# Performance work log

Measured on AMD Instinct MI355X. Metric: run time of the kernel, lower is better.

The kernel has to match this reference:

```python
import jax, jax.numpy as jnp
import numpy as np

N = 50000      # num nodes
E = 500000     # num edges
IN = 128       # in_dim
H = 8          # num_heads
D = 16         # h_dim (out_dim)
CLAMP = 5.0

def setup_inputs() -> dict:
    key = jax.random.key(0)
    ks = jax.random.split(key, 12)
    def xavier(k, shape, fan_in, fan_out):
        std = float(np.sqrt(2.0 / (fan_in + fan_out)))
        return jax.random.normal(k, shape, dtype=jnp.float32) * std
    return {
        "x": jax.random.normal(ks[0], (N, IN), dtype=jnp.float32),
        "edge_attr": jax.random.normal(ks[1], (E, IN), dtype=jnp.float32),
        "edge_index": jax.random.randint(ks[2], (2, E), 0, N, dtype=jnp.int32),
        # Linear weights stored as [in, out] for x @ W + b
        "WQ": xavier(ks[3], (IN, H * D), IN, H * D),
        "bQ": jnp.zeros((H * D,), jnp.float32),
        "WK": xavier(ks[4], (IN, H * D), IN, H * D),
        "bK": jnp.zeros((H * D,), jnp.float32),
        "WE": xavier(ks[5], (IN, 2 * H * D), IN, 2 * H * D),
        "bE": jnp.zeros((2 * H * D,), jnp.float32),
        "WV": xavier(ks[6], (IN, H * D), IN, H * D),
        "bV": jnp.zeros((H * D,), jnp.float32),
        "Aw": xavier(ks[7], (D, H, 1), D, 1),
        "VeRow": xavier(ks[8], (D, H, D), D, D),
    }

def reference(x, edge_attr, edge_index, WQ, bQ, WK, bK, WE, bE, WV, bV, Aw, VeRow):
    src, dst = edge_index[0], edge_index[1]
    Qh = (x @ WQ + bQ).reshape(N, H, D)
    Kh = (x @ WK + bK).reshape(N, H, D)
    Vh = (x @ WV + bV).reshape(N, H, D)
    Ex = (edge_attr @ WE + bE).reshape(E, H, 2 * D)

    # additive score: gathered K/Q plus signed-sqrt edge term
    score1 = Kh[src] + Qh[dst]                       # [E,H,D]
    s2 = Ex[:, :, :D] * Ex[:, :, D:]
    score2 = jnp.sqrt(jax.nn.relu(s2)) - jnp.sqrt(jax.nn.relu(-s2))
    conn = score1 + score2                           # act = Identity

    score = jnp.einsum('ehd,dhc->ehc', conn, Aw)     # [E,H,1]
    score = jnp.clip(score, -CLAMP, CLAMP)

    # scatter-softmax over destination nodes
    m = jax.ops.segment_max(score, dst, num_segments=N)      # [N,H,1]
    ex = jnp.exp(score - m[dst])
    denom = jax.ops.segment_sum(ex, dst, num_segments=N)
    attn = ex / (denom[dst] + 1e-16)                 # [E,H,1]

    # weighted scatter-add aggregation
    msg = Vh[src] * attn                             # [E,H,D]
    Vo = Qh + jax.ops.segment_sum(msg, dst, num_segments=N)
    rowV = jax.ops.segment_sum(conn * attn, dst, num_segments=N)
    Vo = Vo + jnp.einsum('nhd,dhc->nhc', rowV, VeRow)

    return Vo.reshape(N, H * D), conn.reshape(E, H * D)
```

## Files before the change

kernel.cpp:

```cpp
#include <hip/hip_runtime.h>
#include <math.h>

#define N_NODES 50000
#define N_EDGES 500000
#define IN_DIM  128
#define NH      8
#define HD      16
#define OUTD    128
#define CLAMP_V 5.0f

__global__ __launch_bounds__(256) void node_gemm_kernel(
    const float* __restrict__ x,
    const float* __restrict__ WQ, const float* __restrict__ bQ,
    const float* __restrict__ WK, const float* __restrict__ bK,
    const float* __restrict__ WV, const float* __restrict__ bV,
    float* __restrict__ Vo, float* __restrict__ Kh, float* __restrict__ Vh)
{
    __shared__ float A[64][132];
    __shared__ float B[64][64];

    const int t  = threadIdx.x;
    const int bx = blockIdx.x;
    const int by = blockIdx.y;
    const int which = by >> 1;
    const int ch    = (by & 1) * 64;

    const float* W    = (which == 0) ? WQ : (which == 1 ? WK : WV);
    const float* bias = (which == 0) ? bQ : (which == 1 ? bK : bV);
    float*       out  = (which == 0) ? Vo : (which == 1 ? Kh : Vh);

    const int r0 = bx * 64;

    #pragma unroll
    for (int it = 0; it < 8; ++it) {
        int idx = it * 256 + t;
        int k4  = idx & 31;
        int r   = idx >> 5;
        float4 v = make_float4(0.f, 0.f, 0.f, 0.f);
        if (r0 + r < N_NODES)
            v = *(const float4*)(x + (size_t)(r0 + r) * IN_DIM + k4 * 4);
        *(float4*)&A[r][k4 * 4] = v;
    }

    const int tx = t & 15, ty = t >> 4;
    float acc[4][4] = {};

    for (int kh = 0; kh < 2; ++kh) {
        __syncthreads();
        #pragma unroll
        for (int it = 0; it < 4; ++it) {
            int idx = it * 256 + t;
            int c4  = idx & 15;
            int kk  = idx >> 4;
            float4 v = *(const float4*)(W + (size_t)(kh * 64 + kk) * 128 + ch + c4 * 4);
            *(float4*)&B[kk][c4 * 4] = v;
        }
        __syncthreads();

        #pragma unroll 4
        for (int k = 0; k < 64; k += 4) {
            float4 a4[4], b4[4];
            a4[0] = *(const float4*)&A[ty * 4 + 0][kh * 64 + k];
            a4[1] = *(const float4*)&A[ty * 4 + 1][kh * 64 + k];
            a4[2] = *(const float4*)&A[ty * 4 + 2][kh * 64 + k];
            a4[3] = *(const float4*)&A[ty * 4 + 3][kh * 64 + k];
            b4[0] = *(const float4*)&B[k + 0][tx * 4];
            b4[1] = *(const float4*)&B[k + 1][tx * 4];
            b4[2] = *(const float4*)&B[k + 2][tx * 4];
            b4[3] = *(const float4*)&B[k + 3][tx * 4];
            const float* aa = (const float*)a4;
            const float* bb = (const float*)b4;
            #pragma unroll
            for (int kk = 0; kk < 4; ++kk)
                #pragma unroll
                for (int i = 0; i < 4; ++i)
                    #pragma unroll
                    for (int j = 0; j < 4; ++j)
                        acc[i][j] += aa[i * 4 + kk] * bb[kk * 4 + j];
        }
    }

    #pragma unroll
    for (int i = 0; i < 4; ++i) {
        int r = r0 + ty * 4 + i;
        if (r < N_NODES) {
            #pragma unroll
            for (int j = 0; j < 4; ++j) {
                int c = ch + tx * 4 + j;
                out[(size_t)r * OUTD + c] = acc[i][j] + bias[c];
            }
        }
    }
}

__global__ __launch_bounds__(256) void edge_kernel(
    const float* __restrict__ edge_attr,
    const int*   __restrict__ edge_index,
    const float* __restrict__ WE, const float* __restrict__ bE,
    const float* __restrict__ Aw,
    const float* __restrict__ Qh,
    const float* __restrict__ Kh,
    float* __restrict__ conn_out,
    float* __restrict__ exp_s,
    float* __restrict__ denom)
{
    __shared__ float A[64][132];
    __shared__ float B[64][64];

    const int t  = threadIdx.x;
    const int e0 = blockIdx.x * 64;
    const int c0 = blockIdx.y * 64;

    #pragma unroll
    for (int it = 0; it < 8; ++it) {
        int idx = it * 256 + t;
        int k4  = idx & 31;
        int r   = idx >> 5;
        float4 v = make_float4(0.f, 0.f, 0.f, 0.f);
        if (e0 + r < N_EDGES)
            v = *(const float4*)(edge_attr + (size_t)(e0 + r) * IN_DIM + k4 * 4);
        *(float4*)&A[r][k4 * 4] = v;
    }

    const int tx = t & 15, ty = t >> 4;
    float acc[4][4] = {};

    for (int kh = 0; kh < 2; ++kh) {
        __syncthreads();
        #pragma unroll
        for (int it = 0; it < 4; ++it) {
            int idx = it * 256 + t;
            int c4  = idx & 15;
            int kk  = idx >> 4;
            float4 v = *(const float4*)(WE + (size_t)(kh * 64 + kk) * 256 + c0 + c4 * 4);
            *(float4*)&B[kk][c4 * 4] = v;
        }
        __syncthreads();

        #pragma unroll 4
        for (int k = 0; k < 64; k += 4) {
            float4 a4[4], b4[4];
            a4[0] = *(const float4*)&A[ty * 4 + 0][kh * 64 + k];
            a4[1] = *(const float4*)&A[ty * 4 + 1][kh * 64 + k];
            a4[2] = *(const float4*)&A[ty * 4 + 2][kh * 64 + k];
            a4[3] = *(const float4*)&A[ty * 4 + 3][kh * 64 + k];
            b4[0] = *(const float4*)&B[k + 0][tx * 4];
            b4[1] = *(const float4*)&B[k + 1][tx * 4];
            b4[2] = *(const float4*)&B[k + 2][tx * 4];
            b4[3] = *(const float4*)&B[k + 3][tx * 4];
            const float* aa = (const float*)a4;
            const float* bb = (const float*)b4;
            #pragma unroll
            for (int kk = 0; kk < 4; ++kk)
                #pragma unroll
                for (int i = 0; i < 4; ++i)
                    #pragma unroll
                    for (int j = 0; j < 4; ++j)
                        acc[i][j] += aa[i * 4 + kk] * bb[kk * 4 + j];
        }
    }
    __syncthreads();

    #pragma unroll
    for (int i = 0; i < 4; ++i)
        #pragma unroll
        for (int j = 0; j < 4; ++j)
            A[ty * 4 + i][tx * 4 + j] = acc[i][j] + bE[c0 + tx * 4 + j];
    __syncthreads();

    if (t < 128) {
        const int r  = t >> 1;
        const int hl = t & 1;
        const int e  = e0 + r;
        if (e < N_EDGES) {
            const int h   = (c0 >> 5) + hl;
            const int src = edge_index[e];
            const int dst = edge_index[N_EDGES + e];

            const float4* K4 = (const float4*)(Kh + (size_t)src * OUTD + h * HD);
            const float4* Q4 = (const float4*)(Qh + (size_t)dst * OUTD + h * HD);
            float kq[16];
            #pragma unroll
            for (int i = 0; i < 4; ++i) {
                float4 kk = K4[i], qq = Q4[i];
                kq[i * 4 + 0] = kk.x + qq.x;
                kq[i * 4 + 1] = kk.y + qq.y;
                kq[i * 4 + 2] = kk.z + qq.z;
                kq[i * 4 + 3] = kk.w + qq.w;
            }

            float cv[16];
            float score = 0.f;
            #pragma unroll
            for (int d = 0; d < 16; ++d) {
                float s2 = A[r][hl * 32 + d] * A[r][hl * 32 + 16 + d];
                float sq = (s2 >= 0.f) ? sqrtf(s2) : -sqrtf(-s2);
                float c  = kq[d] + sq;
                cv[d] = c;
                score += c * Aw[d * NH + h];
            }
            float4* co = (float4*)(conn_out + (size_t)e * OUTD + h * HD);
            #pragma unroll
            for (int i = 0; i < 4; ++i)
                co[i] = make_float4(cv[i * 4 + 0], cv[i * 4 + 1],
                                    cv[i * 4 + 2], cv[i * 4 + 3]);

            score = fminf(fmaxf(score, -CLAMP_V), CLAMP_V);
            float ex = expf(score);
            exp_s[(size_t)e * NH + h] = ex;
            atomicAdd(&denom[(size_t)dst * NH + h], ex);
        }
    }
}

__global__ __launch_bounds__(256) void scatter_kernel(
    const int*   __restrict__ edge_index,
    const float* __restrict__ Vh,
    const float* __restrict__ conn,
    const float* __restrict__ exp_s,
    const float* __restrict__ denom,
    float* __restrict__ Vo,
    float* __restrict__ rowV)
{
    const int t = threadIdx.x;
    const int e = blockIdx.x * 2 + (t >> 7);
    const int c = t & 127;
    const int h = c >> 4;

    const int src = edge_index[e];
    const int dst = edge_index[N_EDGES + e];

    const float attn = exp_s[(size_t)e * NH + h] /
                       (denom[(size_t)dst * NH + h] + 1e-16f);

    const float mv = Vh[(size_t)src * OUTD + c] * attn;
    atomicAdd(&Vo[(size_t)dst * OUTD + c], mv);
    const float rv = conn[(size_t)e * OUTD + c] * attn;
    atomicAdd(&rowV[(size_t)dst * OUTD + c], rv);
}

__global__ __launch_bounds__(256) void finalize_kernel(
    const float* __restrict__ rowV,
    const float* __restrict__ VeRow,
    float* __restrict__ Vo)
{
    __shared__ float ver[2048];
    __shared__ float rv[256];
    const int t = threadIdx.x;

    #pragma unroll
    for (int it = 0; it < 2; ++it) {
        int idx = it * 256 + t;
        *(float4*)&ver[idx * 4] = *(const float4*)&VeRow[idx * 4];
    }
    const int n0 = blockIdx.x * 2;
    if (t < 64)
        *(float4*)&rv[t * 4] = *(const float4*)&rowV[(size_t)n0 * OUTD + t * 4];
    __syncthreads();

    const int nl = t >> 7, c = t & 127, h = c >> 4, cc = c & 15;
    float acc = 0.f;
    #pragma unroll
    for (int d = 0; d < 16; ++d)
        acc += rv[nl * 128 + h * 16 + d] * ver[d * 128 + h * 16 + cc];

    Vo[(size_t)(n0 + nl) * OUTD + c] += acc;
}

extern "C" void kernel_launch(void* const* d_in, const int* in_sizes, int n_in,
                              void* d_out, int out_size, void* d_ws, size_t ws_size,
                              hipStream_t stream)
{
    const float* x         = (const float*)d_in[0];
    const float* edge_attr = (const float*)d_in[1];
    const int*   edge_index= (const int*)  d_in[2];
    const float* WQ = (const float*)d_in[3];
    const float* bQ = (const float*)d_in[4];
    const float* WK = (const float*)d_in[5];
    const float* bK = (const float*)d_in[6];
    const float* WE = (const float*)d_in[7];
    const float* bE = (const float*)d_in[8];
    const float* WV = (const float*)d_in[9];
    const float* bV = (const float*)d_in[10];
    const float* Aw = (const float*)d_in[11];
    const float* VeRow = (const float*)d_in[12];

    float* Vo   = (float*)d_out;
    float* conn = Vo + (size_t)N_NODES * OUTD;

    float* ws    = (float*)d_ws;
    float* Kh    = ws;
    float* Vh    = Kh   + (size_t)N_NODES * OUTD;
    float* rowV  = Vh   + (size_t)N_NODES * OUTD;
    float* denom = rowV + (size_t)N_NODES * OUTD;
    float* exp_s = denom+ (size_t)N_NODES * NH;

    hipMemsetAsync(rowV,  0, (size_t)N_NODES * OUTD * sizeof(float), stream);
    hipMemsetAsync(denom, 0, (size_t)N_NODES * NH   * sizeof(float), stream);

    dim3 g1((N_NODES + 63) / 64, 6);
    node_gemm_kernel<<<g1, 256, 0, stream>>>(x, WQ, bQ, WK, bK, WV, bV, Vo, Kh, Vh);

    dim3 g2((N_EDGES + 63) / 64, 4);
    edge_kernel<<<g2, 256, 0, stream>>>(edge_attr, edge_index, WE, bE, Aw,
                                        Vo, Kh, conn, exp_s, denom);

    scatter_kernel<<<N_EDGES / 2, 256, 0, stream>>>(edge_index, Vh, conn,
                                                    exp_s, denom, Vo, rowV);

    finalize_kernel<<<N_NODES / 2, 256, 0, stream>>>(rowV, VeRow, Vo);
}
```

Measured before the change: 1.550 ms.

## Use split-bf16 MFMA GEMMs and fuse edge scoring, aggregation and VeRow projection

Replaces the FP32 SIMT GEMMs with MFMA 32x32x16 bf16 GEMMs that use a hi/lo split (three products) to keep near-FP32 accuracy, with weights pre-packed by a small kernel. The edge kernel now covers all 256 edge-projection columns in one block. It also folds the VeRow projection per edge and scatters exp-weighted messages directly, so the scatter and finalize passes and the exp_s/rowV buffers go away. A light final kernel divides by the softmax denominator and adds Q. This trades extra atomics per edge (16 per head) and per-edge VeRow FMAs for removing a full extra pass over conn and Vh gathers. Like before it skips the max subtraction, relying on the clamp.

```diff
diff --git a/kernel.cpp b/kernel.cpp
--- a/kernel.cpp
+++ b/kernel.cpp
@@ -9,177 +9,198 @@
 #define OUTD    128
 #define CLAMP_V 5.0f
 
-__global__ __launch_bounds__(256) void node_gemm_kernel(
+typedef unsigned short ushort_t;
+typedef short bf16x8 __attribute__((ext_vector_type(8)));
+typedef float f32x16 __attribute__((ext_vector_type(16)));
+
+__device__ __forceinline__ ushort_t f2bf(float f) {
+    uint32_t u = __float_as_uint(f);
+    u += 0x7fffu + ((u >> 16) & 1u);
+    return (ushort_t)(u >> 16);
+}
+__device__ __forceinline__ float bf2f(ushort_t h) {
+    return __uint_as_float(((uint32_t)h) << 16);
+}
+
+__device__ __forceinline__ void load_cvt8(const float* p, bool valid,
+                                          bf16x8& hv, bf16x8& lv) {
+    float v[8];
+    if (valid) {
+        float4 a = *(const float4*)p, b = *(const float4*)(p + 4);
+        v[0]=a.x; v[1]=a.y; v[2]=a.z; v[3]=a.w;
+        v[4]=b.x; v[5]=b.y; v[6]=b.z; v[7]=b.w;
+    } else {
+        #pragma unroll
+        for (int j = 0; j < 8; ++j) v[j] = 0.f;
+    }
+    #pragma unroll
+    for (int j = 0; j < 8; ++j) {
+        ushort_t h = f2bf(v[j]);
+        hv[j] = (short)h;
+        lv[j] = (short)f2bf(v[j] - bf2f(h));
+    }
+}
+
+__global__ __launch_bounds__(256) void pack_w_kernel(
+    const float* __restrict__ W, int C,
+    ushort_t* __restrict__ hi, ushort_t* __restrict__ lo)
+{
+    int tid = blockIdx.x * 256 + threadIdx.x;
+    int l  = tid & 63;
+    int ks = (tid >> 6) & 7;
+    int cb = tid >> 9;
+    if (cb * 32 >= C) return;
+    int col = cb * 32 + (l & 31);
+    int k0  = ks * 16 + ((l >> 5) << 3);
+    size_t ob = ((size_t)(cb * 8 + ks) * 64 + l) * 8;
+    #pragma unroll
+    for (int j = 0; j < 8; ++j) {
+        float v = W[(size_t)(k0 + j) * C + col];
+        ushort_t h = f2bf(v);
+        hi[ob + j] = h;
+        lo[ob + j] = f2bf(v - bf2f(h));
+    }
+}
+
+__global__ __launch_bounds__(256) void node_mfma_kernel(
     const float* __restrict__ x,
-    const float* __restrict__ WQ, const float* __restrict__ bQ,
-    const float* __restrict__ WK, const float* __restrict__ bK,
-    const float* __restrict__ WV, const float* __restrict__ bV,
-    float* __restrict__ Vo, float* __restrict__ Kh, float* __restrict__ Vh)
-{
-    __shared__ float A[64][132];
-    __shared__ float B[64][64];
-
-    const int t  = threadIdx.x;
-    const int bx = blockIdx.x;
-    const int by = blockIdx.y;
-    const int which = by >> 1;
-    const int ch    = (by & 1) * 64;
-
-    const float* W    = (which == 0) ? WQ : (which == 1 ? WK : WV);
-    const float* bias = (which == 0) ? bQ : (which == 1 ? bK : bV);
-    float*       out  = (which == 0) ? Vo : (which == 1 ? Kh : Vh);
-
-    const int r0 = bx * 64;
-
-    #pragma unroll
-    for (int it = 0; it < 8; ++it) {
-        int idx = it * 256 + t;
-        int k4  = idx & 31;
-        int r   = idx >> 5;
-        float4 v = make_float4(0.f, 0.f, 0.f, 0.f);
-        if (r0 + r < N_NODES)
-            v = *(const float4*)(x + (size_t)(r0 + r) * IN_DIM + k4 * 4);
-        *(float4*)&A[r][k4 * 4] = v;
-    }
-
-    const int tx = t & 15, ty = t >> 4;
-    float acc[4][4] = {};
-
-    for (int kh = 0; kh < 2; ++kh) {
-        __syncthreads();
-        #pragma unroll
-        for (int it = 0; it < 4; ++it) {
-            int idx = it * 256 + t;
-            int c4  = idx & 15;
-            int kk  = idx >> 4;
-            float4 v = *(const float4*)(W + (size_t)(kh * 64 + kk) * 128 + ch + c4 * 4);
-            *(float4*)&B[kk][c4 * 4] = v;
-        }
-        __syncthreads();
-
-        #pragma unroll 4
-        for (int k = 0; k < 64; k += 4) {
-            float4 a4[4], b4[4];
-            a4[0] = *(const float4*)&A[ty * 4 + 0][kh * 64 + k];
-            a4[1] = *(const float4*)&A[ty * 4 + 1][kh * 64 + k];
-            a4[2] = *(const float4*)&A[ty * 4 + 2][kh * 64 + k];
-            a4[3] = *(const float4*)&A[ty * 4 + 3][kh * 64 + k];
-            b4[0] = *(const float4*)&B[k + 0][tx * 4];
-            b4[1] = *(const float4*)&B[k + 1][tx * 4];
-            b4[2] = *(const float4*)&B[k + 2][tx * 4];
-            b4[3] = *(const float4*)&B[k + 3][tx * 4];
-            const float* aa = (const float*)a4;
-            const float* bb = (const float*)b4;
-            #pragma unroll
-            for (int kk = 0; kk < 4; ++kk)
-                #pragma unroll
-                for (int i = 0; i < 4; ++i)
-                    #pragma unroll
-                    for (int j = 0; j < 4; ++j)
-                        acc[i][j] += aa[i * 4 + kk] * bb[kk * 4 + j];
-        }
-    }
-
-    #pragma unroll
-    for (int i = 0; i < 4; ++i) {
-        int r = r0 + ty * 4 + i;
-        if (r < N_NODES) {
-            #pragma unroll
-            for (int j = 0; j < 4; ++j) {
-                int c = ch + tx * 4 + j;
-                out[(size_t)r * OUTD + c] = acc[i][j] + bias[c];
+    const ushort_t* __restrict__ WQh, const ushort_t* __restrict__ WQl,
+    const ushort_t* __restrict__ WKh, const ushort_t* __restrict__ WKl,
+    const ushort_t* __restrict__ WVh, const ushort_t* __restrict__ WVl,
+    const float* __restrict__ bQ, const float* __restrict__ bK,
+    const float* __restrict__ bV,
+    float* __restrict__ Qs, float* __restrict__ Kn, float* __restrict__ Vn)
+{
+    const int t = threadIdx.x, lane = t & 63, w = t >> 6;
+    const int wi = w >> 1, wjc = w & 1;
+    const int n0 = blockIdx.x * 128;
+    const int which = blockIdx.y;
+    const ushort_t* Whi = (which == 0) ? WQh : (which == 1 ? WKh : WVh);
+    const ushort_t* Wlo = (which == 0) ? WQl : (which == 1 ? WKl : WVl);
+    const float*    bias= (which == 0) ? bQ  : (which == 1 ? bK  : bV);
+    float*          out = (which == 0) ? Qs  : (which == 1 ? Kn  : Vn);
+
+    const int lrow = lane & 31, lk = (lane >> 5) << 3;
+
+    f32x16 acc[2][2];
+    #pragma unroll
+    for (int i = 0; i < 2; ++i)
+        #pragma unroll
+        for (int j = 0; j < 2; ++j)
+            #pragma unroll
+            for (int g = 0; g < 16; ++g) acc[i][j][g] = 0.f;
+
+    #pragma unroll
+    for (int ks = 0; ks < 8; ++ks) {
+        bf16x8 ah[2], al[2];
+        #pragma unroll
+        for (int i = 0; i < 2; ++i) {
+            int row = n0 + wi * 64 + i * 32 + lrow;
+            load_cvt8(x + (size_t)row * IN_DIM + ks * 16 + lk, row < N_NODES,
+                      ah[i], al[i]);
+        }
+        #pragma unroll
+        for (int jf = 0; jf < 2; ++jf) {
+            const int cb = wjc * 2 + jf;
+            size_t ob = ((size_t)(cb * 8 + ks) * 64 + lane) * 8;
+            bf16x8 bh = *(const bf16x8*)(Whi + ob);
+            bf16x8 bl = *(const bf16x8*)(Wlo + ob);
+            #pragma unroll
+            for (int i = 0; i < 2; ++i) {
+                acc[i][jf] = __builtin_amdgcn_mfma_f32_32x32x16_bf16(ah[i], bh, acc[i][jf], 0, 0, 0);
+                acc[i][jf] = __builtin_amdgcn_mfma_f32_32x32x16_bf16(ah[i], bl, acc[i][jf], 0, 0, 0);
+                acc[i][jf] = __builtin_amdgcn_mfma_f32_32x32x16_bf16(al[i], bh, acc[i][jf], 0, 0, 0);
             }
         }
     }
-}
-
-__global__ __launch_bounds__(256) void edge_kernel(
+
+    float bv[2];
+    #pragma unroll
+    for (int jf = 0; jf < 2; ++jf) bv[jf] = bias[wjc * 64 + jf * 32 + lrow];
+
+    #pragma unroll
+    for (int i = 0; i < 2; ++i)
+        #pragma unroll
+        for (int jf = 0; jf < 2; ++jf)
+            #pragma unroll
+            for (int g = 0; g < 16; ++g) {
+                int row = n0 + wi * 64 + i * 32 + (g & 3) + 8 * (g >> 2) + 4 * (lane >> 5);
+                if (row < N_NODES)
+                    out[(size_t)row * OUTD + wjc * 64 + jf * 32 + lrow] = acc[i][jf][g] + bv[jf];
+            }
+}
+
+__global__ __launch_bounds__(256) void edge_mfma_kernel(
     const float* __restrict__ edge_attr,
     const int*   __restrict__ edge_index,
-    const float* __restrict__ WE, const float* __restrict__ bE,
-    const float* __restrict__ Aw,
-    const float* __restrict__ Qh,
-    const float* __restrict__ Kh,
+    const ushort_t* __restrict__ WEh, const ushort_t* __restrict__ WEl,
+    const float* __restrict__ bE, const float* __restrict__ Aw,
+    const float* __restrict__ Qs, const float* __restrict__ Kn,
+    const float* __restrict__ Vn, const float* __restrict__ VeRow,
     float* __restrict__ conn_out,
-    float* __restrict__ exp_s,
+    float* __restrict__ VoAcc,
     float* __restrict__ denom)
 {
-    __shared__ float A[64][132];
-    __shared__ float B[64][64];
-
-    const int t  = threadIdx.x;
+    __shared__ float stash[64 * 256];
+
+    const int t = threadIdx.x, lane = t & 63, w = t >> 6;
+    const int wi = w >> 1, wj = w & 1;
     const int e0 = blockIdx.x * 64;
-    const int c0 = blockIdx.y * 64;
-
-    #pragma unroll
-    for (int it = 0; it < 8; ++it) {
-        int idx = it * 256 + t;
-        int k4  = idx & 31;
-        int r   = idx >> 5;
-        float4 v = make_float4(0.f, 0.f, 0.f, 0.f);
-        if (e0 + r < N_EDGES)
-            v = *(const float4*)(edge_attr + (size_t)(e0 + r) * IN_DIM + k4 * 4);
-        *(float4*)&A[r][k4 * 4] = v;
-    }
-
-    const int tx = t & 15, ty = t >> 4;
-    float acc[4][4] = {};
-
-    for (int kh = 0; kh < 2; ++kh) {
-        __syncthreads();
-        #pragma unroll
-        for (int it = 0; it < 4; ++it) {
-            int idx = it * 256 + t;
-            int c4  = idx & 15;
-            int kk  = idx >> 4;
-            float4 v = *(const float4*)(WE + (size_t)(kh * 64 + kk) * 256 + c0 + c4 * 4);
-            *(float4*)&B[kk][c4 * 4] = v;
-        }
-        __syncthreads();
-
-        #pragma unroll 4
-        for (int k = 0; k < 64; k += 4) {
-            float4 a4[4], b4[4];
-            a4[0] = *(const float4*)&A[ty * 4 + 0][kh * 64 + k];
-            a4[1] = *(const float4*)&A[ty * 4 + 1][kh * 64 + k];
-            a4[2] = *(const float4*)&A[ty * 4 + 2][kh * 64 + k];
-            a4[3] = *(const float4*)&A[ty * 4 + 3][kh * 64 + k];
-            b4[0] = *(const float4*)&B[k + 0][tx * 4];
-            b4[1] = *(const float4*)&B[k + 1][tx * 4];
-            b4[2] = *(const float4*)&B[k + 2][tx * 4];
-            b4[3] = *(const float4*)&B[k + 3][tx * 4];
-            const float* aa = (const float*)a4;
-            const float* bb = (const float*)b4;
-            #pragma unroll
-            for (int kk = 0; kk < 4; ++kk)
-                #pragma unroll
-                for (int i = 0; i < 4; ++i)
-                    #pragma unroll
-                    for (int j = 0; j < 4; ++j)
-                        acc[i][j] += aa[i * 4 + kk] * bb[kk * 4 + j];
-        }
-    }
+
+    const int lrow = lane & 31, lk = (lane >> 5) << 3;
+    const int arow = e0 + wi * 32 + lrow;
+    const bool rvalid = arow < N_EDGES;
+    const float* ap = edge_attr + (size_t)arow * IN_DIM;
+
+    f32x16 acc[4];
+    #pragma unroll
+    for (int jf = 0; jf < 4; ++jf)
+        #pragma unroll
+        for (int g = 0; g < 16; ++g) acc[jf][g] = 0.f;
+
+    #pragma unroll
+    for (int ks = 0; ks < 8; ++ks) {
+        bf16x8 ah, al;
+        load_cvt8(ap + ks * 16 + lk, rvalid, ah, al);
+        #pragma unroll
+        for (int jf = 0; jf < 4; ++jf) {
+            const int cb = wj * 4 + jf;
+            size_t ob = ((size_t)(cb * 8 + ks) * 64 + lane) * 8;
+            bf16x8 bh = *(const bf16x8*)(WEh + ob);
+            bf16x8 bl = *(const bf16x8*)(WEl + ob);
+            acc[jf] = __builtin_amdgcn_mfma_f32_32x32x16_bf16(ah, bh, acc[jf], 0, 0, 0);
+            acc[jf] = __builtin_amdgcn_mfma_f32_32x32x16_bf16(ah, bl, acc[jf], 0, 0, 0);
+            acc[jf] = __builtin_amdgcn_mfma_f32_32x32x16_bf16(al, bh, acc[jf], 0, 0, 0);
+        }
+    }
+
+    float bv[4];
+    #pragma unroll
+    for (int jf = 0; jf < 4; ++jf) bv[jf] = bE[wj * 128 + jf * 32 + lrow];
+    #pragma unroll
+    for (int jf = 0; jf < 4; ++jf)
+        #pragma unroll
+        for (int g = 0; g < 16; ++g) {
+            int r = wi * 32 + (g & 3) + 8 * (g >> 2) + 4 * (lane >> 5);
+            int c = wj * 128 + jf * 32 + lrow;
+            stash[r * 256 + (c ^ (r & 31))] = acc[jf][g] + bv[jf];
+        }
     __syncthreads();
 
-    #pragma unroll
-    for (int i = 0; i < 4; ++i)
-        #pragma unroll
-        for (int j = 0; j < 4; ++j)
-            A[ty * 4 + i][tx * 4 + j] = acc[i][j] + bE[c0 + tx * 4 + j];
-    __syncthreads();
-
-    if (t < 128) {
-        const int r  = t >> 1;
-        const int hl = t & 1;
-        const int e  = e0 + r;
-        if (e < N_EDGES) {
-            const int h   = (c0 >> 5) + hl;
-            const int src = edge_index[e];
-            const int dst = edge_index[N_EDGES + e];
-
-            const float4* K4 = (const float4*)(Kh + (size_t)src * OUTD + h * HD);
-            const float4* Q4 = (const float4*)(Qh + (size_t)dst * OUTD + h * HD);
-            float kq[16];
+    const int r = lane;
+    const int e = e0 + r;
+    const bool valid = e < N_EDGES;
+    const int src = valid ? edge_index[e] : 0;
+    const int dst = valid ? edge_index[N_EDGES + e] : 0;
+
+    #pragma unroll
+    for (int hp = 0; hp < 2; ++hp) {
+        const int h = w + hp * 4;
+
+        float kq[16];
+        {
+            const float4* K4 = (const float4*)(Kn + (size_t)src * OUTD + h * HD);
+            const float4* Q4 = (const float4*)(Qs + (size_t)dst * OUTD + h * HD);
             #pragma unroll
             for (int i = 0; i < 4; ++i) {
                 float4 kk = K4[i], qq = Q4[i];
@@ -188,83 +209,84 @@
                 kq[i * 4 + 2] = kk.z + qq.z;
                 kq[i * 4 + 3] = kk.w + qq.w;
             }
-
-            float cv[16];
-            float score = 0.f;
-            #pragma unroll
-            for (int d = 0; d < 16; ++d) {
-                float s2 = A[r][hl * 32 + d] * A[r][hl * 32 + 16 + d];
-                float sq = (s2 >= 0.f) ? sqrtf(s2) : -sqrtf(-s2);
-                float c  = kq[d] + sq;
-                cv[d] = c;
-                score += c * Aw[d * NH + h];
-            }
+        }
+
+        float cv[16];
+        float score = 0.f;
+        #pragma unroll
+        for (int d = 0; d < 16; ++d) {
+            float x1 = stash[r * 256 + ((h * 32 + d)      ^ (r & 31))];
+            float x2 = stash[r * 256 + ((h * 32 + 16 + d) ^ (r & 31))];
+            float s2 = x1 * x2;
+            float sq = (s2 >= 0.f) ? sqrtf(s2) : -sqrtf(-s2);
+            float c  = kq[d] + sq;
+            cv[d] = c;
+            score += c * Aw[d * NH + h];
+        }
+
+        if (valid) {
             float4* co = (float4*)(conn_out + (size_t)e * OUTD + h * HD);
             #pragma unroll
             for (int i = 0; i < 4; ++i)
                 co[i] = make_float4(cv[i * 4 + 0], cv[i * 4 + 1],
                                     cv[i * 4 + 2], cv[i * 4 + 3]);
-
-            score = fminf(fmaxf(score, -CLAMP_V), CLAMP_V);
-            float ex = expf(score);
-            exp_s[(size_t)e * NH + h] = ex;
-            atomicAdd(&denom[(size_t)dst * NH + h], ex);
-        }
-    }
-}
-
-__global__ __launch_bounds__(256) void scatter_kernel(
-    const int*   __restrict__ edge_index,
-    const float* __restrict__ Vh,
-    const float* __restrict__ conn,
-    const float* __restrict__ exp_s,
-    const float* __restrict__ denom,
-    float* __restrict__ Vo,
-    float* __restrict__ rowV)
-{
-    const int t = threadIdx.x;
-    const int e = blockIdx.x * 2 + (t >> 7);
-    const int c = t & 127;
-    const int h = c >> 4;
-
-    const int src = edge_index[e];
-    const int dst = edge_index[N_EDGES + e];
-
-    const float attn = exp_s[(size_t)e * NH + h] /
-                       (denom[(size_t)dst * NH + h] + 1e-16f);
-
-    const float mv = Vh[(size_t)src * OUTD + c] * attn;
-    atomicAdd(&Vo[(size_t)dst * OUTD + c], mv);
-    const float rv = conn[(size_t)e * OUTD + c] * attn;
-    atomicAdd(&rowV[(size_t)dst * OUTD + c], rv);
-}
-
-__global__ __launch_bounds__(256) void finalize_kernel(
-    const float* __restrict__ rowV,
-    const float* __restrict__ VeRow,
+        }
+
+        score = fminf(fmaxf(score, -CLAMP_V), CLAMP_V);
+        const float ex = __expf(score);
+
+        float outv[16];
+        {
+            const float4* V4 = (const float4*)(Vn + (size_t)src * OUTD + h * HD);
+            #pragma unroll
+            for (int i = 0; i < 4; ++i) {
+                float4 vv = V4[i];
+                outv[i * 4 + 0] = vv.x; outv[i * 4 + 1] = vv.y;
+                outv[i * 4 + 2] = vv.z; outv[i * 4 + 3] = vv.w;
+            }
+        }
+        #pragma unroll
+        for (int d = 0; d < 16; ++d) {
+            const float4* vr = (const float4*)(VeRow + d * OUTD + h * HD);
+            float cvd = cv[d];
+            float4 v0 = vr[0], v1 = vr[1], v2 = vr[2], v3 = vr[3];
+            outv[0]  += cvd * v0.x; outv[1]  += cvd * v0.y;
+            outv[2]  += cvd * v0.z; outv[3]  += cvd * v0.w;
+            outv[4]  += cvd * v1.x; outv[5]  += cvd * v1.y;
+            outv[6]  += cvd * v1.z; outv[7]  += cvd * v1.w;
+            outv[8]  += cvd * v2.x; outv[9]  += cvd * v2.y;
+            outv[10] += cvd * v2.z; outv[11] += cvd * v2.w;
+            outv[12] += cvd * v3.x; outv[13] += cvd * v3.y;
+            outv[14] += cvd * v3.z; outv[15] += cvd * v3.w;
+        }
+
+        if (valid) {
+            atomicAdd(denom + (size_t)dst * NH + h, ex);
+            float* vp = VoAcc + (size_t)dst * OUTD + h * HD;
+            #pragma unroll
+            for (int c = 0; c < 16; ++c)
+                atomicAdd(vp + c, ex * outv[c]);
+        }
+    }
+}
+
+__global__ __launch_bounds__(256) void final_kernel(
+    const float* __restrict__ Qs, const float* __restrict__ denom,
     float* __restrict__ Vo)
 {
-    __shared__ float ver[2048];
-    __shared__ float rv[256];
-    const int t = threadIdx.x;
-
-    #pragma unroll
-    for (int it = 0; it < 2; ++it) {
-        int idx = it * 256 + t;
-        *(float4*)&ver[idx * 4] = *(const float4*)&VeRow[idx * 4];
-    }
-    const int n0 = blockIdx.x * 2;
-    if (t < 64)
-        *(float4*)&rv[t * 4] = *(const float4*)&rowV[(size_t)n0 * OUTD + t * 4];
-    __syncthreads();
-
-    const int nl = t >> 7, c = t & 127, h = c >> 4, cc = c & 15;
-    float acc = 0.f;
-    #pragma unroll
-    for (int d = 0; d < 16; ++d)
-        acc += rv[nl * 128 + h * 16 + d] * ver[d * 128 + h * 16 + cc];
-
-    Vo[(size_t)(n0 + nl) * OUTD + c] += acc;
+    int idx = blockIdx.x * 256 + threadIdx.x;
+    if (idx >= N_NODES * 32) return;
+    int n  = idx >> 5;
+    int c4 = (idx & 31) * 4;
+    int h  = c4 >> 4;
+    float inv = 1.f / (denom[(size_t)n * NH + h] + 1e-16f);
+    float4 a = *(float4*)(Vo + (size_t)n * OUTD + c4);
+    const float4 q = *(const float4*)(Qs + (size_t)n * OUTD + c4);
+    a.x = q.x + a.x * inv;
+    a.y = q.y + a.y * inv;
+    a.z = q.z + a.z * inv;
+    a.w = q.w + a.w * inv;
+    *(float4*)(Vo + (size_t)n * OUTD + c4) = a;
 }
 
 extern "C" void kernel_launch(void* const* d_in, const int* in_sizes, int n_in,
@@ -289,24 +311,35 @@
     float* conn = Vo + (size_t)N_NODES * OUTD;
 
     float* ws    = (float*)d_ws;
-    float* Kh    = ws;
-    float* Vh    = Kh   + (size_t)N_NODES * OUTD;
-    float* rowV  = Vh   + (size_t)N_NODES * OUTD;
-    float* denom = rowV + (size_t)N_NODES * OUTD;
-    float* exp_s = denom+ (size_t)N_NODES * NH;
-
-    hipMemsetAsync(rowV,  0, (size_t)N_NODES * OUTD * sizeof(float), stream);
+    float* Qs    = ws;
+    float* Kn    = Qs + (size_t)N_NODES * OUTD;
+    float* Vn    = Kn + (size_t)N_NODES * OUTD;
+    float* denom = Vn + (size_t)N_NODES * OUTD;
+    ushort_t* WQh = (ushort_t*)(denom + (size_t)N_NODES * NH);
+    ushort_t* WQl = WQh + 16384;
+    ushort_t* WKh = WQl + 16384;
+    ushort_t* WKl = WKh + 16384;
+    ushort_t* WVh = WKl + 16384;
+    ushort_t* WVl = WVh + 16384;
+    ushort_t* WEh = WVl + 16384;
+    ushort_t* WEl = WEh + 32768;
+
+    hipMemsetAsync(Vo,    0, (size_t)N_NODES * OUTD * sizeof(float), stream);
     hipMemsetAsync(denom, 0, (size_t)N_NODES * NH   * sizeof(float), stream);
 
-    dim3 g1((N_NODES + 63) / 64, 6);
-    node_gemm_kernel<<<g1, 256, 0, stream>>>(x, WQ, bQ, WK, bK, WV, bV, Vo, Kh, Vh);
-
-    dim3 g2((N_EDGES + 63) / 64, 4);
-    edge_kernel<<<g2, 256, 0, stream>>>(edge_attr, edge_index, WE, bE, Aw,
-                                        Vo, Kh, conn, exp_s, denom);
-
-    scatter_kernel<<<N_EDGES / 2, 256, 0, stream>>>(edge_index, Vh, conn,
-                                                    exp_s, denom, Vo, rowV);
-
-    finalize_kernel<<<N_NODES / 2, 256, 0, stream>>>(rowV, VeRow, Vo);
-}
+    pack_w_kernel<<<8,  256, 0, stream>>>(WQ, 128, WQh, WQl);
+    pack_w_kernel<<<8,  256, 0, stream>>>(WK, 128, WKh, WKl);
+    pack_w_kernel<<<8,  256, 0, stream>>>(WV, 128, WVh, WVl);
+    pack_w_kernel<<<16, 256, 0, stream>>>(WE, 256, WEh, WEl);
+
+    dim3 g1((N_NODES + 127) / 128, 3);
+    node_mfma_kernel<<<g1, 256, 0, stream>>>(x, WQh, WQl, WKh, WKl, WVh, WVl,
+                                             bQ, bK, bV, Qs, Kn, Vn);
+
+    const int nblk = (N_EDGES + 63) / 64;
+    edge_mfma_kernel<<<nblk, 256, 0, stream>>>(edge_attr, edge_index, WEh, WEl,
+                                               bE, Aw, Qs, Kn, Vn, VeRow,
+                                               conn, Vo, denom);
+
+    final_kernel<<<(N_NODES * 32 + 255) / 256, 256, 0, stream>>>(Qs, denom, Vo);
+}
```

Result: slower. 4.134 ms (+166.7%).
